# Kernel optimization log

Measured on AMD Instinct MI355X. Metric: run time of the kernel, lower is better.

Reference implementation:

```python
import jax, jax.numpy as jnp
import numpy as np

H = 128

def setup_inputs() -> dict:
    key = jax.random.key(0)
    ks = jax.random.split(key, 7)
    x = jax.random.normal(ks[0], (4, 65536, H), dtype=jnp.float32)
    # Linear(3H -> H) and Linear(H -> H), torch-style fan-in init scale
    W1 = jax.random.normal(ks[1], (3 * H, H), dtype=jnp.float32) / np.sqrt(3 * H)
    b1 = jax.random.normal(ks[2], (H,), dtype=jnp.float32) * 0.01
    W2 = jax.random.normal(ks[3], (H, H), dtype=jnp.float32) / np.sqrt(H)
    b2 = jax.random.normal(ks[4], (H,), dtype=jnp.float32) * 0.01
    gamma = jnp.ones((H,), dtype=jnp.float32)
    beta = jnp.zeros((H,), dtype=jnp.float32)
    return {"x": x, "W1": W1, "b1": b1, "W2": W2, "b2": b2, "gamma": gamma, "beta": beta}


def _layernorm(h, gamma, beta, eps=1e-5):
    mu = jnp.mean(h, axis=-1, keepdims=True)
    var = jnp.var(h, axis=-1, keepdims=True)
    return (h - mu) * jax.lax.rsqrt(var + eps) * gamma + beta


def reference(x, W1, b1, W2, b2, gamma, beta):
    # circular neighbor gather along node dim
    prev_x = jnp.roll(x, 1, axis=1)
    next_x = jnp.roll(x, -1, axis=1)
    cat = jnp.concatenate([prev_x, x, next_x], axis=-1)  # [B, N, 3H]
    h = jax.nn.relu(jnp.einsum('bnc,ch->bnh', cat, W1) + b1)
    delta = jnp.einsum('bnh,hk->bnk', h, W2) + b2
    return jax.nn.relu(_layernorm(x + delta, gamma, beta))
```

## Files before the change

kernel.cpp:

```cpp
#include <hip/hip_runtime.h>


typedef __bf16 bf16x8 __attribute__((ext_vector_type(8)));
typedef __bf16 bf16x4 __attribute__((ext_vector_type(4)));
typedef float  f32x4  __attribute__((ext_vector_type(4)));

#define H      128
#define NB     65536
#define TILE   64
#define XS     136
#define HSS    136
#define PSS    18
#define NTILES 4096
#define GRID   512

__global__ __launch_bounds__(256, 2)
void cbb_kernel(const float* __restrict__ x, const float* __restrict__ W1,
                const float* __restrict__ b1, const float* __restrict__ W2,
                const float* __restrict__ b2, const float* __restrict__ gamma,
                const float* __restrict__ beta, float* __restrict__ out) {
    __shared__ __align__(16) char raw[(66 * XS + 64 * HSS) * 2];
    __bf16* xs = (__bf16*)raw;
    __bf16* hs = xs + 66 * XS;
    __shared__ __align__(16) __bf16 w2s[16384];
    __shared__ __align__(16) float2 ps2[64 * PSS];
    __shared__ __align__(16) float s_b1[128], s_b2[128], s_gamma[128], s_beta[128];

    const int tid  = threadIdx.x;
    const int wid  = tid >> 6;
    const int lane = tid & 63;
    const int l    = lane & 15;
    const int g    = lane >> 4;
    const int col0 = wid * 32;

    if (tid < 128) {
        s_b1[tid] = b1[tid];   s_b2[tid]   = b2[tid];
        s_gamma[tid] = gamma[tid]; s_beta[tid] = beta[tid];
    }

    bf16x8 w1f[12][2];
#pragma unroll
    for (int ks = 0; ks < 12; ++ks) {
#pragma unroll
        for (int ct = 0; ct < 2; ++ct) {
            const int cc = col0 + ct * 16 + l;
            bf16x8 f;
#pragma unroll
            for (int j = 0; j < 8; ++j)
                f[j] = (__bf16)W1[(ks * 32 + g * 8 + j) * H + cc];
            w1f[ks][ct] = f;
        }
    }

    for (int idx = tid; idx < 16384; idx += 256) {
        const int j  = idx & 7;
        const int ln = (idx >> 3) & 63;
        const int ct = (idx >> 9) & 1;
        const int ks = (idx >> 10) & 3;
        const int w  = idx >> 12;
        const int row = ks * 32 + (ln >> 4) * 8 + j;
        const int col = w * 32 + ct * 16 + (ln & 15);
        w2s[idx] = (__bf16)W2[row * H + col];
    }
    const __bf16* w2w = w2s + wid * 4096;

    float4 xreg[8];
    float4 xhalo;
    {
        const int t  = blockIdx.x;
        const int b  = t >> 10;
        const int n0 = (t & 1023) << 6;
        const size_t rowbase = (size_t)b * NB;
#pragma unroll
        for (int s = 0; s < 8; ++s) {
            const int q = tid + s * 256;
            const int r = q >> 5, c = q & 31;
            const int grow = (n0 - 1 + r + NB) & (NB - 1);
            xreg[s] = *(const float4*)(x + ((rowbase + grow) * H + c * 4));
        }
        if (tid < 64) {
            const int q = 2048 + tid;
            const int r = q >> 5, c = q & 31;
            const int grow = (n0 - 1 + r + NB) & (NB - 1);
            xhalo = *(const float4*)(x + ((rowbase + grow) * H + c * 4));
        }
    }

    for (int t = blockIdx.x; t < NTILES; t += GRID) {
        const int b  = t >> 10;
        const int n0 = (t & 1023) << 6;
        const size_t rowbase = (size_t)b * NB;


#pragma unroll
        for (int s = 0; s < 8; ++s) {
            const int q = tid + s * 256;
            const int r = q >> 5, c = q & 31;
            bf16x4 v4;
            v4[0] = (__bf16)xreg[s].x; v4[1] = (__bf16)xreg[s].y;
            v4[2] = (__bf16)xreg[s].z; v4[3] = (__bf16)xreg[s].w;
            *(bf16x4*)(xs + r * XS + c * 4) = v4;
        }
        if (tid < 64) {
            const int q = 2048 + tid;
            const int r = q >> 5, c = q & 31;
            bf16x4 v4;
            v4[0] = (__bf16)xhalo.x; v4[1] = (__bf16)xhalo.y;
            v4[2] = (__bf16)xhalo.z; v4[3] = (__bf16)xhalo.w;
            *(bf16x4*)(xs + r * XS + c * 4) = v4;
        }
        __syncthreads();

        if (t + GRID < NTILES) {
            const int tn  = t + GRID;
            const int bn  = tn >> 10;
            const int n0n = (tn & 1023) << 6;
            const size_t rbn = (size_t)bn * NB;
#pragma unroll
            for (int s = 0; s < 8; ++s) {
                const int q = tid + s * 256;
                const int r = q >> 5, c = q & 31;
                const int grow = (n0n - 1 + r + NB) & (NB - 1);
                xreg[s] = *(const float4*)(x + ((rbn + grow) * H + c * 4));
            }
            if (tid < 64) {
                const int q = 2048 + tid;
                const int r = q >> 5, c = q & 31;
                const int grow = (n0n - 1 + r + NB) & (NB - 1);
                xhalo = *(const float4*)(x + ((rbn + grow) * H + c * 4));
            }
        }

        f32x4 acc[4][2];
#pragma unroll
        for (int rt = 0; rt < 4; ++rt)
#pragma unroll
            for (int ct = 0; ct < 2; ++ct)
                acc[rt][ct] = (f32x4){0.f, 0.f, 0.f, 0.f};

        __builtin_amdgcn_s_setprio(1);
#pragma unroll
        for (int ks = 0; ks < 12; ++ks) {
            const int k  = ks * 32 + g * 8;
            const int ro = k >> 7, kc = k & 127;
#pragma unroll
            for (int rt = 0; rt < 4; ++rt) {
                const bf16x8 a = *(const bf16x8*)(xs + (rt * 16 + l + ro) * XS + kc);
                acc[rt][0] = __builtin_amdgcn_mfma_f32_16x16x32_bf16(w1f[ks][0], a, acc[rt][0], 0, 0, 0);
                acc[rt][1] = __builtin_amdgcn_mfma_f32_16x16x32_bf16(w1f[ks][1], a, acc[rt][1], 0, 0, 0);
            }
        }
        __builtin_amdgcn_s_setprio(0);

        {
            const f32x4 b1q0 = *(const f32x4*)(s_b1 + col0 + g * 4);
            const f32x4 b1q1 = *(const f32x4*)(s_b1 + col0 + 16 + g * 4);
#pragma unroll
            for (int rt = 0; rt < 4; ++rt) {
                bf16x4 h0, h1;
#pragma unroll
                for (int i = 0; i < 4; ++i) {
                    h0[i] = (__bf16)fmaxf(acc[rt][0][i] + b1q0[i], 0.f);
                    h1[i] = (__bf16)fmaxf(acc[rt][1][i] + b1q1[i], 0.f);
                }
                *(bf16x4*)(hs + (rt * 16 + l) * HSS + col0 + g * 4)      = h0;
                *(bf16x4*)(hs + (rt * 16 + l) * HSS + col0 + 16 + g * 4) = h1;
            }
        }
        __syncthreads();

        f32x4 acc2[4][2];
#pragma unroll
        for (int rt = 0; rt < 4; ++rt)
#pragma unroll
            for (int ct = 0; ct < 2; ++ct)
                acc2[rt][ct] = (f32x4){0.f, 0.f, 0.f, 0.f};

        __builtin_amdgcn_s_setprio(1);
#pragma unroll
        for (int ks = 0; ks < 4; ++ks) {
            const bf16x8 wf0 = *(const bf16x8*)(w2w + ks * 1024 + lane * 8);
            const bf16x8 wf1 = *(const bf16x8*)(w2w + ks * 1024 + 512 + lane * 8);
#pragma unroll
            for (int rt = 0; rt < 4; ++rt) {
                const bf16x8 a = *(const bf16x8*)(hs + (rt * 16 + l) * HSS + ks * 32 + g * 8);
                acc2[rt][0] = __builtin_amdgcn_mfma_f32_16x16x32_bf16(wf0, a, acc2[rt][0], 0, 0, 0);
                acc2[rt][1] = __builtin_amdgcn_mfma_f32_16x16x32_bf16(wf1, a, acc2[rt][1], 0, 0, 0);
            }
        }
        __builtin_amdgcn_s_setprio(0);

        {
            const f32x4 b2q0 = *(const f32x4*)(s_b2 + col0 + g * 4);
            const f32x4 b2q1 = *(const f32x4*)(s_b2 + col0 + 16 + g * 4);
#pragma unroll
            for (int rt = 0; rt < 4; ++rt) {
                const bf16x4 xv0 = *(const bf16x4*)(xs + (rt * 16 + l + 1) * XS + col0 + g * 4);
                const bf16x4 xv1 = *(const bf16x4*)(xs + (rt * 16 + l + 1) * XS + col0 + 16 + g * 4);
#pragma unroll
                for (int i = 0; i < 4; ++i) {
                    acc2[rt][0][i] += b2q0[i] + (float)xv0[i];
                    acc2[rt][1][i] += b2q1[i] + (float)xv1[i];
                }
            }
        }

#pragma unroll
        for (int rt = 0; rt < 4; ++rt) {
            float s = 0.f, qq = 0.f;
#pragma unroll
            for (int ct = 0; ct < 2; ++ct)
#pragma unroll
                for (int i = 0; i < 4; ++i) {
                    const float v = acc2[rt][ct][i];
                    s += v; qq += v * v;
                }
            ps2[(rt * 16 + l) * PSS + wid * 4 + g] = make_float2(s, qq);
        }
        __syncthreads();

        float mu, rv;
        {
            const f32x4* pp = (const f32x4*)(ps2 + lane * PSS);
            float S = 0.f, Q = 0.f;
#pragma unroll
            for (int j = 0; j < 4; ++j) {
                const f32x4 e0 = pp[2 * j];
                const f32x4 e1 = pp[2 * j + 1];
                S += (e0[0] + e0[2]) + (e1[0] + e1[2]);
                Q += (e0[1] + e0[3]) + (e1[1] + e1[3]);
            }
            mu = S * (1.f / 128.f);
            const float var = Q * (1.f / 128.f) - mu * mu;
            rv = rsqrtf(var + 1e-5f);
        }

        {
            const f32x4 gm0 = *(const f32x4*)(s_gamma + col0 + g * 4);
            const f32x4 gm1 = *(const f32x4*)(s_gamma + col0 + 16 + g * 4);
            const f32x4 bt0 = *(const f32x4*)(s_beta + col0 + g * 4);
            const f32x4 bt1 = *(const f32x4*)(s_beta + col0 + 16 + g * 4);
#pragma unroll
            for (int rt = 0; rt < 4; ++rt) {
                const float mur = __shfl(mu, (lane & 15) + rt * 16);
                const float rvr = __shfl(rv, (lane & 15) + rt * 16);
                float* op = out + (rowbase + n0 + rt * 16 + l) * H + col0;
                f32x4 o0, o1;
#pragma unroll
                for (int i = 0; i < 4; ++i) {
                    o0[i] = fmaxf((acc2[rt][0][i] - mur) * rvr * gm0[i] + bt0[i], 0.f);
                    o1[i] = fmaxf((acc2[rt][1][i] - mur) * rvr * gm1[i] + bt1[i], 0.f);
                }
                *(f32x4*)(op + g * 4)      = o0;
                *(f32x4*)(op + 16 + g * 4) = o1;
            }
        }
    }
}

extern "C" void kernel_launch(void* const* d_in, const int* in_sizes, int n_in,
                              void* d_out, int out_size, void* d_ws, size_t ws_size,
                              hipStream_t stream) {
    const float* x     = (const float*)d_in[0];
    const float* W1    = (const float*)d_in[1];
    const float* b1    = (const float*)d_in[2];
    const float* W2    = (const float*)d_in[3];
    const float* b2    = (const float*)d_in[4];
    const float* gamma = (const float*)d_in[5];
    const float* beta  = (const float*)d_in[6];
    float* out = (float*)d_out;

    cbb_kernel<<<GRID, 256, 0, stream>>>(x, W1, b1, W2, b2, gamma, beta, out);
}
```

Measured before the change: 261.1 us.

## Defer LayerNorm epilogue stores to next tile iteration for overlap

The final normalize, ReLU and global store for each tile now runs at the start of the next tile iteration, after the next tile's x is written to LDS, with a drain after the loop. The aim is to overlap the output stores with the next tile's MFMA work instead of ending each iteration on a store-bound tail. The accumulators, mean and rstd stay live in registers across the loop, which raises register pressure under launch_bounds(256,2) and may cause spills.

```diff
diff --git a/kernel.cpp b/kernel.cpp
--- a/kernel.cpp
+++ b/kernel.cpp
@@ -86,6 +86,10 @@
         }
     }
 
+    f32x4 dacc[4][2];
+    float dmu = 0.f, drv = 0.f;
+    float* dop = nullptr;
+
     for (int t = blockIdx.x; t < NTILES; t += GRID) {
         const int b  = t >> 10;
         const int n0 = (t & 1023) << 6;
@@ -131,6 +135,27 @@
             }
         }
 
+        if (dop) {
+            const f32x4 gm0 = *(const f32x4*)(s_gamma + col0 + g * 4);
+            const f32x4 gm1 = *(const f32x4*)(s_gamma + col0 + 16 + g * 4);
+            const f32x4 bt0 = *(const f32x4*)(s_beta + col0 + g * 4);
+            const f32x4 bt1 = *(const f32x4*)(s_beta + col0 + 16 + g * 4);
+#pragma unroll
+            for (int rt = 0; rt < 4; ++rt) {
+                const float mur = __shfl(dmu, (lane & 15) + rt * 16);
+                const float rvr = __shfl(drv, (lane & 15) + rt * 16);
+                float* op = dop + (rt * 16 + l) * H + col0;
+                f32x4 o0, o1;
+#pragma unroll
+                for (int i = 0; i < 4; ++i) {
+                    o0[i] = fmaxf((dacc[rt][0][i] - mur) * rvr * gm0[i] + bt0[i], 0.f);
+                    o1[i] = fmaxf((dacc[rt][1][i] - mur) * rvr * gm1[i] + bt1[i], 0.f);
+                }
+                *(f32x4*)(op + g * 4)      = o0;
+                *(f32x4*)(op + 16 + g * 4) = o1;
+            }
+        }
+
         f32x4 acc[4][2];
 #pragma unroll
         for (int rt = 0; rt < 4; ++rt)
@@ -169,12 +194,11 @@
         }
         __syncthreads();
 
-        f32x4 acc2[4][2];
 #pragma unroll
         for (int rt = 0; rt < 4; ++rt)
 #pragma unroll
             for (int ct = 0; ct < 2; ++ct)
-                acc2[rt][ct] = (f32x4){0.f, 0.f, 0.f, 0.f};
+                dacc[rt][ct] = (f32x4){0.f, 0.f, 0.f, 0.f};
 
         __builtin_amdgcn_s_setprio(1);
 #pragma unroll
@@ -184,8 +208,8 @@
 #pragma unroll
             for (int rt = 0; rt < 4; ++rt) {
                 const bf16x8 a = *(const bf16x8*)(hs + (rt * 16 + l) * HSS + ks * 32 + g * 8);
-                acc2[rt][0] = __builtin_amdgcn_mfma_f32_16x16x32_bf16(wf0, a, acc2[rt][0], 0, 0, 0);
-                acc2[rt][1] = __builtin_amdgcn_mfma_f32_16x16x32_bf16(wf1, a, acc2[rt][1], 0, 0, 0);
+                dacc[rt][0] = __builtin_amdgcn_mfma_f32_16x16x32_bf16(wf0, a, dacc[rt][0], 0, 0, 0);
+                dacc[rt][1] = __builtin_amdgcn_mfma_f32_16x16x32_bf16(wf1, a, dacc[rt][1], 0, 0, 0);
             }
         }
         __builtin_amdgcn_s_setprio(0);
@@ -199,8 +223,8 @@
                 const bf16x4 xv1 = *(const bf16x4*)(xs + (rt * 16 + l + 1) * XS + col0 + 16 + g * 4);
 #pragma unroll
                 for (int i = 0; i < 4; ++i) {
-                    acc2[rt][0][i] += b2q0[i] + (float)xv0[i];
-                    acc2[rt][1][i] += b2q1[i] + (float)xv1[i];
+                    dacc[rt][0][i] += b2q0[i] + (float)xv0[i];
+                    dacc[rt][1][i] += b2q1[i] + (float)xv1[i];
                 }
             }
         }
@@ -212,14 +236,13 @@
             for (int ct = 0; ct < 2; ++ct)
 #pragma unroll
                 for (int i = 0; i < 4; ++i) {
-                    const float v = acc2[rt][ct][i];
+                    const float v = dacc[rt][ct][i];
                     s += v; qq += v * v;
                 }
             ps2[(rt * 16 + l) * PSS + wid * 4 + g] = make_float2(s, qq);
         }
         __syncthreads();
 
-        float mu, rv;
         {
             const f32x4* pp = (const f32x4*)(ps2 + lane * PSS);
             float S = 0.f, Q = 0.f;
@@ -230,30 +253,31 @@
                 S += (e0[0] + e0[2]) + (e1[0] + e1[2]);
                 Q += (e0[1] + e0[3]) + (e1[1] + e1[3]);
             }
-            mu = S * (1.f / 128.f);
-            const float var = Q * (1.f / 128.f) - mu * mu;
-            rv = rsqrtf(var + 1e-5f);
-        }
-
-        {
-            const f32x4 gm0 = *(const f32x4*)(s_gamma + col0 + g * 4);
-            const f32x4 gm1 = *(const f32x4*)(s_gamma + col0 + 16 + g * 4);
-            const f32x4 bt0 = *(const f32x4*)(s_beta + col0 + g * 4);
-            const f32x4 bt1 = *(const f32x4*)(s_beta + col0 + 16 + g * 4);
-#pragma unroll
-            for (int rt = 0; rt < 4; ++rt) {
-                const float mur = __shfl(mu, (lane & 15) + rt * 16);
-                const float rvr = __shfl(rv, (lane & 15) + rt * 16);
-                float* op = out + (rowbase + n0 + rt * 16 + l) * H + col0;
-                f32x4 o0, o1;
-#pragma unroll
-                for (int i = 0; i < 4; ++i) {
-                    o0[i] = fmaxf((acc2[rt][0][i] - mur) * rvr * gm0[i] + bt0[i], 0.f);
-                    o1[i] = fmaxf((acc2[rt][1][i] - mur) * rvr * gm1[i] + bt1[i], 0.f);
-                }
-                *(f32x4*)(op + g * 4)      = o0;
-                *(f32x4*)(op + 16 + g * 4) = o1;
-            }
+            dmu = S * (1.f / 128.f);
+            const float var = Q * (1.f / 128.f) - dmu * dmu;
+            drv = rsqrtf(var + 1e-5f);
+            dop = out + (rowbase + n0) * H;
+        }
+    }
+
+    if (dop) {
+        const f32x4 gm0 = *(const f32x4*)(s_gamma + col0 + g * 4);
+        const f32x4 gm1 = *(const f32x4*)(s_gamma + col0 + 16 + g * 4);
+        const f32x4 bt0 = *(const f32x4*)(s_beta + col0 + g * 4);
+        const f32x4 bt1 = *(const f32x4*)(s_beta + col0 + 16 + g * 4);
+#pragma unroll
+        for (int rt = 0; rt < 4; ++rt) {
+            const float mur = __shfl(dmu, (lane & 15) + rt * 16);
+            const float rvr = __shfl(drv, (lane & 15) + rt * 16);
+            float* op = dop + (rt * 16 + l) * H + col0;
+            f32x4 o0, o1;
+#pragma unroll
+            for (int i = 0; i < 4; ++i) {
+                o0[i] = fmaxf((dacc[rt][0][i] - mur) * rvr * gm0[i] + bt0[i], 0.f);
+                o1[i] = fmaxf((dacc[rt][1][i] - mur) * rvr * gm1[i] + bt1[i], 0.f);
+            }
+            *(f32x4*)(op + g * 4)      = o0;
+            *(f32x4*)(op + 16 + g * 4) = o1;
         }
     }
 }
```

Measured after the change: 269.7 us. +3.3%, slower.

## Read x fragments directly from global memory instead of staging in LDS

Applied to the files above, without the earlier changes.

Removes the shared-memory x tile, its register prefetch of the next tile, and the associated barrier. The GEMM1 A-fragments are loaded straight from global memory as fp32 and converted to bf16 in registers, and the residual add now reads fp32 x directly. The aim is to cut LDS traffic and free LDS for occupancy. In exchange, each row is read three times from global or L2 (prev, cur, next), and the software prefetch that overlapped loads with compute is lost, so load latency sits on the MFMA critical path.

```diff
diff --git a/kernel.cpp b/kernel.cpp
--- a/kernel.cpp
+++ b/kernel.cpp
@@ -8,7 +8,6 @@
 #define H      128
 #define NB     65536
 #define TILE   64
-#define XS     136
 #define HSS    136
 #define PSS    18
 #define NTILES 4096
@@ -19,9 +18,7 @@
                 const float* __restrict__ b1, const float* __restrict__ W2,
                 const float* __restrict__ b2, const float* __restrict__ gamma,
                 const float* __restrict__ beta, float* __restrict__ out) {
-    __shared__ __align__(16) char raw[(66 * XS + 64 * HSS) * 2];
-    __bf16* xs = (__bf16*)raw;
-    __bf16* hs = xs + 66 * XS;
+    __shared__ __align__(16) __bf16 hs[64 * HSS];
     __shared__ __align__(16) __bf16 w2s[16384];
     __shared__ __align__(16) float2 ps2[64 * PSS];
     __shared__ __align__(16) float s_b1[128], s_b2[128], s_gamma[128], s_beta[128];
@@ -63,74 +60,13 @@
         w2s[idx] = (__bf16)W2[row * H + col];
     }
     const __bf16* w2w = w2s + wid * 4096;
-
-    float4 xreg[8];
-    float4 xhalo;
-    {
-        const int t  = blockIdx.x;
-        const int b  = t >> 10;
-        const int n0 = (t & 1023) << 6;
-        const size_t rowbase = (size_t)b * NB;
-#pragma unroll
-        for (int s = 0; s < 8; ++s) {
-            const int q = tid + s * 256;
-            const int r = q >> 5, c = q & 31;
-            const int grow = (n0 - 1 + r + NB) & (NB - 1);
-            xreg[s] = *(const float4*)(x + ((rowbase + grow) * H + c * 4));
-        }
-        if (tid < 64) {
-            const int q = 2048 + tid;
-            const int r = q >> 5, c = q & 31;
-            const int grow = (n0 - 1 + r + NB) & (NB - 1);
-            xhalo = *(const float4*)(x + ((rowbase + grow) * H + c * 4));
-        }
-    }
+    __syncthreads();
 
     for (int t = blockIdx.x; t < NTILES; t += GRID) {
         const int b  = t >> 10;
         const int n0 = (t & 1023) << 6;
         const size_t rowbase = (size_t)b * NB;
 
-
-#pragma unroll
-        for (int s = 0; s < 8; ++s) {
-            const int q = tid + s * 256;
-            const int r = q >> 5, c = q & 31;
-            bf16x4 v4;
-            v4[0] = (__bf16)xreg[s].x; v4[1] = (__bf16)xreg[s].y;
-            v4[2] = (__bf16)xreg[s].z; v4[3] = (__bf16)xreg[s].w;
-            *(bf16x4*)(xs + r * XS + c * 4) = v4;
-        }
-        if (tid < 64) {
-            const int q = 2048 + tid;
-            const int r = q >> 5, c = q & 31;
-            bf16x4 v4;
-            v4[0] = (__bf16)xhalo.x; v4[1] = (__bf16)xhalo.y;
-            v4[2] = (__bf16)xhalo.z; v4[3] = (__bf16)xhalo.w;
-            *(bf16x4*)(xs + r * XS + c * 4) = v4;
-        }
-        __syncthreads();
-
-        if (t + GRID < NTILES) {
-            const int tn  = t + GRID;
-            const int bn  = tn >> 10;
-            const int n0n = (tn & 1023) << 6;
-            const size_t rbn = (size_t)bn * NB;
-#pragma unroll
-            for (int s = 0; s < 8; ++s) {
-                const int q = tid + s * 256;
-                const int r = q >> 5, c = q & 31;
-                const int grow = (n0n - 1 + r + NB) & (NB - 1);
-                xreg[s] = *(const float4*)(x + ((rbn + grow) * H + c * 4));
-            }
-            if (tid < 64) {
-                const int q = 2048 + tid;
-                const int r = q >> 5, c = q & 31;
-                const int grow = (n0n - 1 + r + NB) & (NB - 1);
-                xhalo = *(const float4*)(x + ((rbn + grow) * H + c * 4));
-            }
-        }
-
         f32x4 acc[4][2];
 #pragma unroll
         for (int rt = 0; rt < 4; ++rt)
@@ -141,11 +77,19 @@
         __builtin_amdgcn_s_setprio(1);
 #pragma unroll
         for (int ks = 0; ks < 12; ++ks) {
-            const int k  = ks * 32 + g * 8;
-            const int ro = k >> 7, kc = k & 127;
-#pragma unroll
-            for (int rt = 0; rt < 4; ++rt) {
-                const bf16x8 a = *(const bf16x8*)(xs + (rt * 16 + l + ro) * XS + kc);
+            const int kc = (ks & 3) * 32 + g * 8;
+            const int dr = (ks >> 2) - 1;
+#pragma unroll
+            for (int rt = 0; rt < 4; ++rt) {
+                const int row = (n0 + rt * 16 + l + dr + NB) & (NB - 1);
+                const float* p = x + (rowbase + row) * H + kc;
+                const float4 fa = *(const float4*)p;
+                const float4 fb = *(const float4*)(p + 4);
+                bf16x8 a;
+                a[0] = (__bf16)fa.x; a[1] = (__bf16)fa.y;
+                a[2] = (__bf16)fa.z; a[3] = (__bf16)fa.w;
+                a[4] = (__bf16)fb.x; a[5] = (__bf16)fb.y;
+                a[6] = (__bf16)fb.z; a[7] = (__bf16)fb.w;
                 acc[rt][0] = __builtin_amdgcn_mfma_f32_16x16x32_bf16(w1f[ks][0], a, acc[rt][0], 0, 0, 0);
                 acc[rt][1] = __builtin_amdgcn_mfma_f32_16x16x32_bf16(w1f[ks][1], a, acc[rt][1], 0, 0, 0);
             }
@@ -195,12 +139,13 @@
             const f32x4 b2q1 = *(const f32x4*)(s_b2 + col0 + 16 + g * 4);
 #pragma unroll
             for (int rt = 0; rt < 4; ++rt) {
-                const bf16x4 xv0 = *(const bf16x4*)(xs + (rt * 16 + l + 1) * XS + col0 + g * 4);
-                const bf16x4 xv1 = *(const bf16x4*)(xs + (rt * 16 + l + 1) * XS + col0 + 16 + g * 4);
-#pragma unroll
-                for (int i = 0; i < 4; ++i) {
-                    acc2[rt][0][i] += b2q0[i] + (float)xv0[i];
-                    acc2[rt][1][i] += b2q1[i] + (float)xv1[i];
+                const float* xr = x + (rowbase + n0 + rt * 16 + l) * H + col0;
+                const f32x4 xv0 = *(const f32x4*)(xr + g * 4);
+                const f32x4 xv1 = *(const f32x4*)(xr + 16 + g * 4);
+#pragma unroll
+                for (int i = 0; i < 4; ++i) {
+                    acc2[rt][0][i] += b2q0[i] + xv0[i];
+                    acc2[rt][1][i] += b2q1[i] + xv1[i];
                 }
             }
         }
```

New measurement: 422.8 us. 1.62x slower.
